# Performance work log

Measured on AMD Instinct MI355X. Metric: run time of the kernel, lower is better.

The kernel has to match this reference:

```python
import jax, jax.numpy as jnp
import numpy as np

B, S, D = 4, 4096, 200


def setup_inputs() -> dict:
    key = jax.random.key(0)
    ks = jax.random.split(key, 10)
    sc = 1.0 / np.sqrt(D)
    return {
        "modal1_input": jax.random.normal(ks[0], (B, S, D), dtype=jnp.float32),
        "modal2_input": jax.random.normal(ks[1], (B, S, D), dtype=jnp.float32),
        "Wq": jax.random.normal(ks[2], (D, D), dtype=jnp.float32) * sc,
        "bq": jnp.zeros((D,), dtype=jnp.float32),
        "Wk": jax.random.normal(ks[3], (D, D), dtype=jnp.float32) * sc,
        "bk": jnp.zeros((D,), dtype=jnp.float32),
        "Wv": jax.random.normal(ks[4], (D, D), dtype=jnp.float32) * sc,
        "bv": jnp.zeros((D,), dtype=jnp.float32),
        "Wo": jax.random.normal(ks[5], (D, D), dtype=jnp.float32) * sc,
        "bo": jnp.zeros((D,), dtype=jnp.float32),
    }


def _self_attend(x, Wq, bq, Wk, bk, Wv, bv):
    # torch nn.Linear: y = x @ W.T + b
    q = x @ Wq.T + bq  # [B,S,D]
    k = x @ Wk.T + bk
    v = x @ Wv.T + bv
    scale = 1.0 / jnp.sqrt(jnp.asarray(q.shape[-1], q.dtype))
    scores = jnp.einsum("bsd,btd->bst", q, k) * scale  # [B,S,S]
    w = jax.nn.softmax(scores, axis=-1)
    return jnp.einsum("bst,btd->bsd", w, v)


def reference(modal1_input, modal2_input, Wq, bq, Wk, bk, Wv, bv, Wo, bo):
    a1 = _self_attend(modal1_input, Wq, bq, Wk, bk, Wv, bv)
    a2 = _self_attend(modal2_input, Wq, bq, Wk, bk, Wv, bv)
    fused = a1 + a2
    return fused @ Wo.T + bo
```

## Files before the change

kernel.cpp:

```cpp
#include <hip/hip_runtime.h>

#define SLEN 4096
#define DIM  200
#define DP   224
#define DPL  232
#define VD   208
#define VTL  72
#define HKV  2048

typedef __bf16 bf16t;
typedef bf16t bf16x8 __attribute__((ext_vector_type(8)));
typedef float f32x4 __attribute__((ext_vector_type(4)));

static __device__ __forceinline__ f32x4 mfma16(bf16x8 a, bf16x8 b, f32x4 c) {
    return __builtin_amdgcn_mfma_f32_16x16x32_bf16(a, b, c, 0, 0, 0);
}

static __device__ __forceinline__ unsigned short f2bf(float f) {
    unsigned int u = __float_as_uint(f);
    u += 0x7FFFu + ((u >> 16) & 1u);
    return (unsigned short)(u >> 16);
}

static __device__ __forceinline__ float bf2f(unsigned short s) {
    return __uint_as_float((unsigned)s << 16);
}

static __device__ __forceinline__ uint2 pack4(float a, float b, float c, float d) {
    uint2 r;
    r.x = (unsigned)f2bf(a) | ((unsigned)f2bf(b) << 16);
    r.y = (unsigned)f2bf(c) | ((unsigned)f2bf(d) << 16);
    return r;
}

__global__ __launch_bounds__(256, 2)
void proj_kernel(const float* __restrict__ x1, const float* __restrict__ x2,
                 const float* __restrict__ Wq, const float* __restrict__ bq,
                 const float* __restrict__ Wk, const float* __restrict__ bk,
                 const float* __restrict__ Wv, const float* __restrict__ bv,
                 unsigned short* __restrict__ Qg, unsigned short* __restrict__ Kg,
                 unsigned short* __restrict__ Vtg)
{
    __shared__ unsigned short x_lds[64 * DPL];
    __shared__ unsigned short w_lds[64 * DPL];
    __shared__ unsigned short vt_lds[64 * 66];

    const int tid = threadIdx.x;
    const int mod = blockIdx.x >> 8;
    const int rb  = blockIdx.x & 255;
    const int r0  = rb * 64;
    const int bidx = r0 >> 12;
    const int s0  = r0 & 4095;
    const int unit = mod * 4 + bidx;
    const float* __restrict__ x = mod ? x2 : x1;

    for (int i = tid; i < 3200; i += 256) {
        int r = i / 50, c = i % 50;
        const float4 v = *(const float4*)(x + (size_t)(r0 + r) * DIM + c * 4);
        *(uint2*)(x_lds + r * DPL + c * 4) = pack4(v.x, v.y, v.z, v.w);
    }
    {
        int r = tid >> 2, c4 = tid & 3;
        uint2 z = make_uint2(0u, 0u);
        *(uint2*)(x_lds + r * DPL + 200 + c4 * 4) = z;
        *(uint2*)(x_lds + r * DPL + 216 + c4 * 4) = z;
        *(uint2*)(w_lds + r * DPL + 200 + c4 * 4) = z;
        *(uint2*)(w_lds + r * DPL + 216 + c4 * 4) = z;
    }
    __syncthreads();

    const int wv = tid >> 6, lane = tid & 63, ln = lane & 15, h = lane >> 4;

    bf16x8 afrag[7];
    #pragma unroll
    for (int kk = 0; kk < 7; ++kk)
        afrag[kk] = *(const bf16x8*)(x_lds + (wv * 16 + ln) * DPL + kk * 32 + 8 * h);

    for (int mmat = 0; mmat < 3; ++mmat) {
        const float* W  = (mmat == 0) ? Wq : (mmat == 1 ? Wk : Wv);
        const float* bi = (mmat == 0) ? bq : (mmat == 1 ? bk : bv);
        for (int t = 0; t < 4; ++t) {
            for (int i = tid; i < 3200; i += 256) {
                int r = i / 50, c = i % 50;
                int og = t * 64 + r;
                uint2 val = make_uint2(0u, 0u);
                if (og < DIM) {
                    const float4 v = *(const float4*)(W + (size_t)og * DIM + c * 4);
                    val = pack4(v.x, v.y, v.z, v.w);
                }
                *(uint2*)(w_lds + r * DPL + c * 4) = val;
            }
            __syncthreads();

            f32x4 acc[4];
            #pragma unroll
            for (int sub = 0; sub < 4; ++sub) acc[sub] = (f32x4){0.f, 0.f, 0.f, 0.f};
            #pragma unroll
            for (int kk = 0; kk < 7; ++kk) {
                #pragma unroll
                for (int sub = 0; sub < 4; ++sub) {
                    bf16x8 bfrag = *(const bf16x8*)(w_lds + (sub * 16 + ln) * DPL + kk * 32 + 8 * h);
                    acc[sub] = mfma16(afrag[kk], bfrag, acc[sub]);
                }
            }

            if (mmat < 2) {
                unsigned short* dst = (mmat == 0) ? Qg : Kg;
                #pragma unroll
                for (int sub = 0; sub < 4; ++sub) {
                    int og = t * 64 + sub * 16 + ln;
                    if (og < DIM) {
                        float bias = bi[og];
                        #pragma unroll
                        for (int r = 0; r < 4; ++r) {
                            int srow = s0 + wv * 16 + 4 * h + r;
                            dst[((size_t)unit * SLEN + srow) * DP + og] = f2bf(acc[sub][r] + bias);
                        }
                    }
                }
                __syncthreads();
            } else {
                #pragma unroll
                for (int sub = 0; sub < 4; ++sub) {
                    int og = t * 64 + sub * 16 + ln;
                    float bias = (og < DIM) ? bi[og] : 0.f;
                    #pragma unroll
                    for (int r = 0; r < 4; ++r) {
                        float val = (og < DIM) ? (acc[sub][r] + bias) : 0.f;
                        vt_lds[(wv * 16 + 4 * h + r) * 66 + sub * 16 + ln] = f2bf(val);
                    }
                }
                __syncthreads();
                for (int p = 0; p < 2; ++p) {
                    int idx = p * 256 + tid;
                    int dl = idx >> 3, cc = idx & 7;
                    int og = t * 64 + dl;
                    if (og < VD) {
                        unsigned short tmp[8];
                        #pragma unroll
                        for (int j = 0; j < 8; ++j)
                            tmp[j] = vt_lds[(cc * 8 + j) * 66 + dl];
                        *(uint4*)(Vtg + ((size_t)unit * VD + og) * SLEN + s0 + cc * 8) = *(uint4*)tmp;
                    }
                }
                __syncthreads();
            }
        }
    }
}

__global__ __launch_bounds__(512, 4)
void attn_kernel(const unsigned short* __restrict__ Qg,
                 const unsigned short* __restrict__ Kg,
                 const unsigned short* __restrict__ Vtg,
                 unsigned short* __restrict__ Ap,
                 float2* __restrict__ Mlg)
{
    __shared__ unsigned short k_lds[64 * DPL];
    __shared__ unsigned short vt_lds[VD * VTL];
    __shared__ unsigned short p_lds[8 * 16 * VTL];

    const int tid = threadIdx.x;
    const int u   = blockIdx.x & 7;
    const int qt  = (blockIdx.x >> 3) & 31;
    const int hf  = blockIdx.x >> 8;
    const int wv = tid >> 6, lane = tid & 63, ln = lane & 15, h = lane >> 4;
    const size_t ubase = (size_t)u * SLEN;

    bf16x8 qfrag[7];
    {
        const size_t qoff = (ubase + qt * 128 + wv * 16 + ln) * DP;
        #pragma unroll
        for (int kk = 0; kk < 7; ++kk)
            qfrag[kk] = *(const bf16x8*)(Qg + qoff + kk * 32 + 8 * h);
    }

    float mrun[4], lrun[4];
    #pragma unroll
    for (int r = 0; r < 4; ++r) { mrun[r] = -1e30f; lrun[r] = 0.f; }
    f32x4 acc[13];
    #pragma unroll
    for (int d = 0; d < 13; ++d) acc[d] = (f32x4){0.f, 0.f, 0.f, 0.f};

    const float scale = 0.07071067811865475f;
    const int t_beg = hf * HKV;

    for (int t0 = t_beg; t0 < t_beg + HKV; t0 += 64) {
        #pragma unroll
        for (int it = 0; it < 4; ++it) {
            int i = it * 512 + tid;
            if (i < 1792) {
                int r = i / 28, c = i % 28;
                *(uint4*)(k_lds + r * DPL + c * 8) =
                    *(const uint4*)(Kg + (ubase + t0 + r) * DP + c * 8);
            }
            if (i < 1664) {
                int r = i >> 3, c = i & 7;
                *(uint4*)(vt_lds + r * VTL + c * 8) =
                    *(const uint4*)(Vtg + ((size_t)u * VD + r) * SLEN + t0 + c * 8);
            }
        }
        __syncthreads();

        f32x4 sc[4];
        #pragma unroll
        for (int sub = 0; sub < 4; ++sub) sc[sub] = (f32x4){0.f, 0.f, 0.f, 0.f};
        #pragma unroll
        for (int kk = 0; kk < 7; ++kk) {
            #pragma unroll
            for (int sub = 0; sub < 4; ++sub) {
                bf16x8 bfrag = *(const bf16x8*)(k_lds + (sub * 16 + ln) * DPL + kk * 32 + 8 * h);
                sc[sub] = mfma16(qfrag[kk], bfrag, sc[sub]);
            }
        }

        float mxs[4];
        #pragma unroll
        for (int r = 0; r < 4; ++r) {
            float mx = fmaxf(fmaxf(sc[0][r], sc[1][r]), fmaxf(sc[2][r], sc[3][r]));
            mx = fmaxf(mx, __shfl_xor(mx, 1));
            mx = fmaxf(mx, __shfl_xor(mx, 2));
            mx = fmaxf(mx, __shfl_xor(mx, 4));
            mx = fmaxf(mx, __shfl_xor(mx, 8));
            mxs[r] = mx * scale;
        }

        int need = (mxs[0] > mrun[0] + 8.f) | (mxs[1] > mrun[1] + 8.f) |
                   (mxs[2] > mrun[2] + 8.f) | (mxs[3] > mrun[3] + 8.f);
        if (__any(need)) {
            #pragma unroll
            for (int r = 0; r < 4; ++r) {
                float mnew = fmaxf(mrun[r], mxs[r]);
                float alpha = __expf(mrun[r] - mnew);
                lrun[r] *= alpha;
                #pragma unroll
                for (int d = 0; d < 13; ++d) acc[d][r] *= alpha;
                mrun[r] = mnew;
            }
        }

        #pragma unroll
        for (int r = 0; r < 4; ++r) {
            float rsum = 0.f;
            #pragma unroll
            for (int sub = 0; sub < 4; ++sub) {
                float p = __expf(sc[sub][r] * scale - mrun[r]);
                rsum += p;
                p_lds[wv * (16 * VTL) + (4 * h + r) * VTL + sub * 16 + ln] = f2bf(p);
            }
            rsum += __shfl_xor(rsum, 1);
            rsum += __shfl_xor(rsum, 2);
            rsum += __shfl_xor(rsum, 4);
            rsum += __shfl_xor(rsum, 8);
            lrun[r] += rsum;
        }

        #pragma unroll
        for (int ks = 0; ks < 2; ++ks) {
            bf16x8 pfrag = *(const bf16x8*)(p_lds + wv * (16 * VTL) + ln * VTL + ks * 32 + 8 * h);
            #pragma unroll
            for (int d = 0; d < 13; ++d) {
                bf16x8 bfrag = *(const bf16x8*)(vt_lds + (d * 16 + ln) * VTL + ks * 32 + 8 * h);
                acc[d] = mfma16(pfrag, bfrag, acc[d]);
            }
        }
        __syncthreads();
    }

    const int slab = hf * 8 + u;
    unsigned short* Adst = Ap + (size_t)slab * SLEN * VD;
    #pragma unroll
    for (int r = 0; r < 4; ++r) {
        int srow = qt * 128 + wv * 16 + 4 * h + r;
        #pragma unroll
        for (int d = 0; d < 13; ++d)
            Adst[(size_t)srow * VD + d * 16 + ln] = f2bf(acc[d][r]);
        if (ln == 0)
            Mlg[(size_t)slab * SLEN + srow] = make_float2(mrun[r], lrun[r]);
    }
}

__global__ __launch_bounds__(256, 2)
void out_kernel(const unsigned short* __restrict__ Ap,
                const float2* __restrict__ Mlg,
                const float* __restrict__ Wo,
                const float* __restrict__ bo, float* __restrict__ out)
{
    __shared__ unsigned short a_lds[64 * DPL];
    __shared__ unsigned short w_lds[64 * DPL];

    const int tid = threadIdx.x;
    const int r0 = blockIdx.x * 64;
    const int bidx = r0 >> 12;
    const int s0 = r0 & 4095;

    const unsigned short* A1a = Ap + (size_t)(bidx)      * SLEN * VD;
    const unsigned short* A1b = Ap + (size_t)(8 + bidx)  * SLEN * VD;
    const unsigned short* A2a = Ap + (size_t)(4 + bidx)  * SLEN * VD;
    const unsigned short* A2b = Ap + (size_t)(12 + bidx) * SLEN * VD;
    const float2* M1a = Mlg + (size_t)(bidx)      * SLEN;
    const float2* M1b = Mlg + (size_t)(8 + bidx)  * SLEN;
    const float2* M2a = Mlg + (size_t)(4 + bidx)  * SLEN;
    const float2* M2b = Mlg + (size_t)(12 + bidx) * SLEN;

    for (int i = tid; i < 3200; i += 256) {
        int r = i / 50, c = i % 50;
        int srow = s0 + r;
        size_t off = (size_t)srow * VD + c * 4;

        float2 ml1a = M1a[srow], ml1b = M1b[srow];
        float2 ml2a = M2a[srow], ml2b = M2b[srow];
        float M1 = fmaxf(ml1a.x, ml1b.x);
        float w1a = __expf(ml1a.x - M1), w1b = __expf(ml1b.x - M1);
        float inv1 = 1.f / (ml1a.y * w1a + ml1b.y * w1b);
        float M2 = fmaxf(ml2a.x, ml2b.x);
        float w2a = __expf(ml2a.x - M2), w2b = __expf(ml2b.x - M2);
        float inv2 = 1.f / (ml2a.y * w2a + ml2b.y * w2b);

        uint2 pa = *(const uint2*)(A1a + off);
        uint2 pb = *(const uint2*)(A1b + off);
        uint2 qa = *(const uint2*)(A2a + off);
        uint2 qb = *(const uint2*)(A2b + off);

        float f[4];
        f[0] = (bf2f((unsigned short)(pa.x & 0xffff)) * w1a + bf2f((unsigned short)(pb.x & 0xffff)) * w1b) * inv1
             + (bf2f((unsigned short)(qa.x & 0xffff)) * w2a + bf2f((unsigned short)(qb.x & 0xffff)) * w2b) * inv2;
        f[1] = (bf2f((unsigned short)(pa.x >> 16))    * w1a + bf2f((unsigned short)(pb.x >> 16))    * w1b) * inv1
             + (bf2f((unsigned short)(qa.x >> 16))    * w2a + bf2f((unsigned short)(qb.x >> 16))    * w2b) * inv2;
        f[2] = (bf2f((unsigned short)(pa.y & 0xffff)) * w1a + bf2f((unsigned short)(pb.y & 0xffff)) * w1b) * inv1
             + (bf2f((unsigned short)(qa.y & 0xffff)) * w2a + bf2f((unsigned short)(qb.y & 0xffff)) * w2b) * inv2;
        f[3] = (bf2f((unsigned short)(pa.y >> 16))    * w1a + bf2f((unsigned short)(pb.y >> 16))    * w1b) * inv1
             + (bf2f((unsigned short)(qa.y >> 16))    * w2a + bf2f((unsigned short)(qb.y >> 16))    * w2b) * inv2;

        *(uint2*)(a_lds + r * DPL + c * 4) = pack4(f[0], f[1], f[2], f[3]);
    }
    {
        int r = tid >> 2, c4 = tid & 3;
        uint2 z = make_uint2(0u, 0u);
        *(uint2*)(a_lds + r * DPL + 200 + c4 * 4) = z;
        *(uint2*)(a_lds + r * DPL + 216 + c4 * 4) = z;
        *(uint2*)(w_lds + r * DPL + 200 + c4 * 4) = z;
        *(uint2*)(w_lds + r * DPL + 216 + c4 * 4) = z;
    }
    __syncthreads();

    const int wv = tid >> 6, lane = tid & 63, ln = lane & 15, h = lane >> 4;
    bf16x8 afrag[7];
    #pragma unroll
    for (int kk = 0; kk < 7; ++kk)
        afrag[kk] = *(const bf16x8*)(a_lds + (wv * 16 + ln) * DPL + kk * 32 + 8 * h);

    for (int t = 0; t < 4; ++t) {
        for (int i = tid; i < 3200; i += 256) {
            int r = i / 50, c = i % 50;
            int og = t * 64 + r;
            uint2 val = make_uint2(0u, 0u);
            if (og < DIM) {
                const float4 v = *(const float4*)(Wo + (size_t)og * DIM + c * 4);
                val = pack4(v.x, v.y, v.z, v.w);
            }
            *(uint2*)(w_lds + r * DPL + c * 4) = val;
        }
        __syncthreads();

        f32x4 acc[4];
        #pragma unroll
        for (int sub = 0; sub < 4; ++sub) acc[sub] = (f32x4){0.f, 0.f, 0.f, 0.f};
        #pragma unroll
        for (int kk = 0; kk < 7; ++kk) {
            #pragma unroll
            for (int sub = 0; sub < 4; ++sub) {
                bf16x8 bfrag = *(const bf16x8*)(w_lds + (sub * 16 + ln) * DPL + kk * 32 + 8 * h);
                acc[sub] = mfma16(afrag[kk], bfrag, acc[sub]);
            }
        }

        #pragma unroll
        for (int sub = 0; sub < 4; ++sub) {
            int og = t * 64 + sub * 16 + ln;
            if (og < DIM) {
                float bias = bo[og];
                #pragma unroll
                for (int r = 0; r < 4; ++r) {
                    int row = r0 + wv * 16 + 4 * h + r;
                    out[(size_t)row * DIM + og] = acc[sub][r] + bias;
                }
            }
        }
        __syncthreads();
    }
}

extern "C" void kernel_launch(void* const* d_in, const int* in_sizes, int n_in,
                              void* d_out, int out_size, void* d_ws, size_t ws_size,
                              hipStream_t stream)
{
    const float* x1 = (const float*)d_in[0];
    const float* x2 = (const float*)d_in[1];
    const float* Wq = (const float*)d_in[2];
    const float* bq = (const float*)d_in[3];
    const float* Wk = (const float*)d_in[4];
    const float* bk = (const float*)d_in[5];
    const float* Wv = (const float*)d_in[6];
    const float* bv = (const float*)d_in[7];
    const float* Wo = (const float*)d_in[8];
    const float* bo = (const float*)d_in[9];

    unsigned short* Qg  = (unsigned short*)d_ws;
    unsigned short* Kg  = Qg + (size_t)8 * SLEN * DP;
    unsigned short* Vtg = Kg + (size_t)8 * SLEN * DP;
    unsigned short* Apg = Vtg + (size_t)8 * VD * SLEN;
    float2*         Mlg = (float2*)(Apg + (size_t)16 * SLEN * VD);

    proj_kernel<<<dim3(512), dim3(256), 0, stream>>>(x1, x2, Wq, bq, Wk, bk, Wv, bv,
                                                     Qg, Kg, Vtg);
    attn_kernel<<<dim3(512), dim3(512), 0, stream>>>(Qg, Kg, Vtg, Apg, Mlg);
    out_kernel<<<dim3(256), dim3(256), 0, stream>>>(Apg, Mlg, Wo, bo, (float*)d_out);
}
```

Baseline: 409.1 us.

## Give each attention wave two query tiles and precompute combine weights in out kernel

The attention kernel now runs 256 threads per block, and each wave handles 32 query rows as two 16-row MFMA tiles. Each K and V fragment read from LDS is reused across both tiles, halving LDS reads per MFMA. The cost is roughly double the accumulator and Q-fragment registers, plus fewer waves per block to hide latency. The output kernel now computes the per-row softmax combine weights once into shared memory and loads the attention partials with 16-byte reads instead of 8-byte reads.

```diff
diff --git a/kernel.cpp b/kernel.cpp
--- a/kernel.cpp
+++ b/kernel.cpp
@@ -149,7 +149,7 @@
     }
 }
 
-__global__ __launch_bounds__(512, 4)
+__global__ __launch_bounds__(256, 2)
 void attn_kernel(const unsigned short* __restrict__ Qg,
                  const unsigned short* __restrict__ Kg,
                  const unsigned short* __restrict__ Vtg,
@@ -158,7 +158,7 @@
 {
     __shared__ unsigned short k_lds[64 * DPL];
     __shared__ unsigned short vt_lds[VD * VTL];
-    __shared__ unsigned short p_lds[8 * 16 * VTL];
+    __shared__ unsigned short p_lds[128 * VTL];
 
     const int tid = threadIdx.x;
     const int u   = blockIdx.x & 7;
@@ -167,29 +167,34 @@
     const int wv = tid >> 6, lane = tid & 63, ln = lane & 15, h = lane >> 4;
     const size_t ubase = (size_t)u * SLEN;
 
-    bf16x8 qfrag[7];
-    {
-        const size_t qoff = (ubase + qt * 128 + wv * 16 + ln) * DP;
+    bf16x8 qfrag[2][7];
+    #pragma unroll
+    for (int mt = 0; mt < 2; ++mt) {
+        const size_t qoff = (ubase + qt * 128 + wv * 32 + mt * 16 + ln) * DP;
         #pragma unroll
         for (int kk = 0; kk < 7; ++kk)
-            qfrag[kk] = *(const bf16x8*)(Qg + qoff + kk * 32 + 8 * h);
-    }
-
-    float mrun[4], lrun[4];
-    #pragma unroll
-    for (int r = 0; r < 4; ++r) { mrun[r] = -1e30f; lrun[r] = 0.f; }
-    f32x4 acc[13];
-    #pragma unroll
-    for (int d = 0; d < 13; ++d) acc[d] = (f32x4){0.f, 0.f, 0.f, 0.f};
+            qfrag[mt][kk] = *(const bf16x8*)(Qg + qoff + kk * 32 + 8 * h);
+    }
+
+    float mrun[2][4], lrun[2][4];
+    #pragma unroll
+    for (int mt = 0; mt < 2; ++mt)
+        #pragma unroll
+        for (int r = 0; r < 4; ++r) { mrun[mt][r] = -1e30f; lrun[mt][r] = 0.f; }
+    f32x4 acc[2][13];
+    #pragma unroll
+    for (int mt = 0; mt < 2; ++mt)
+        #pragma unroll
+        for (int d = 0; d < 13; ++d) acc[mt][d] = (f32x4){0.f, 0.f, 0.f, 0.f};
 
     const float scale = 0.07071067811865475f;
     const int t_beg = hf * HKV;
 
     for (int t0 = t_beg; t0 < t_beg + HKV; t0 += 64) {
         #pragma unroll
-        for (int it = 0; it < 4; ++it) {
-            int i = it * 512 + tid;
-            if (i < 1792) {
+        for (int it = 0; it < 7; ++it) {
+            int i = it * 256 + tid;
+            {
                 int r = i / 28, c = i % 28;
                 *(uint4*)(k_lds + r * DPL + c * 8) =
                     *(const uint4*)(Kg + (ubase + t0 + r) * DP + c * 8);
@@ -202,66 +207,75 @@
         }
         __syncthreads();
 
-        f32x4 sc[4];
-        #pragma unroll
-        for (int sub = 0; sub < 4; ++sub) sc[sub] = (f32x4){0.f, 0.f, 0.f, 0.f};
+        f32x4 sc[2][4];
+        #pragma unroll
+        for (int mt = 0; mt < 2; ++mt)
+            #pragma unroll
+            for (int sub = 0; sub < 4; ++sub) sc[mt][sub] = (f32x4){0.f, 0.f, 0.f, 0.f};
         #pragma unroll
         for (int kk = 0; kk < 7; ++kk) {
             #pragma unroll
             for (int sub = 0; sub < 4; ++sub) {
                 bf16x8 bfrag = *(const bf16x8*)(k_lds + (sub * 16 + ln) * DPL + kk * 32 + 8 * h);
-                sc[sub] = mfma16(qfrag[kk], bfrag, sc[sub]);
-            }
-        }
-
-        float mxs[4];
-        #pragma unroll
-        for (int r = 0; r < 4; ++r) {
-            float mx = fmaxf(fmaxf(sc[0][r], sc[1][r]), fmaxf(sc[2][r], sc[3][r]));
-            mx = fmaxf(mx, __shfl_xor(mx, 1));
-            mx = fmaxf(mx, __shfl_xor(mx, 2));
-            mx = fmaxf(mx, __shfl_xor(mx, 4));
-            mx = fmaxf(mx, __shfl_xor(mx, 8));
-            mxs[r] = mx * scale;
-        }
-
-        int need = (mxs[0] > mrun[0] + 8.f) | (mxs[1] > mrun[1] + 8.f) |
-                   (mxs[2] > mrun[2] + 8.f) | (mxs[3] > mrun[3] + 8.f);
-        if (__any(need)) {
+                sc[0][sub] = mfma16(qfrag[0][kk], bfrag, sc[0][sub]);
+                sc[1][sub] = mfma16(qfrag[1][kk], bfrag, sc[1][sub]);
+            }
+        }
+
+        #pragma unroll
+        for (int mt = 0; mt < 2; ++mt) {
+            float mxs[4];
             #pragma unroll
             for (int r = 0; r < 4; ++r) {
-                float mnew = fmaxf(mrun[r], mxs[r]);
-                float alpha = __expf(mrun[r] - mnew);
-                lrun[r] *= alpha;
-                #pragma unroll
-                for (int d = 0; d < 13; ++d) acc[d][r] *= alpha;
-                mrun[r] = mnew;
-            }
-        }
-
-        #pragma unroll
-        for (int r = 0; r < 4; ++r) {
-            float rsum = 0.f;
-            #pragma unroll
-            for (int sub = 0; sub < 4; ++sub) {
-                float p = __expf(sc[sub][r] * scale - mrun[r]);
-                rsum += p;
-                p_lds[wv * (16 * VTL) + (4 * h + r) * VTL + sub * 16 + ln] = f2bf(p);
-            }
-            rsum += __shfl_xor(rsum, 1);
-            rsum += __shfl_xor(rsum, 2);
-            rsum += __shfl_xor(rsum, 4);
-            rsum += __shfl_xor(rsum, 8);
-            lrun[r] += rsum;
+                float mx = fmaxf(fmaxf(sc[mt][0][r], sc[mt][1][r]),
+                                 fmaxf(sc[mt][2][r], sc[mt][3][r]));
+                mx = fmaxf(mx, __shfl_xor(mx, 1));
+                mx = fmaxf(mx, __shfl_xor(mx, 2));
+                mx = fmaxf(mx, __shfl_xor(mx, 4));
+                mx = fmaxf(mx, __shfl_xor(mx, 8));
+                mxs[r] = mx * scale;
+            }
+
+            int need = (mxs[0] > mrun[mt][0] + 8.f) | (mxs[1] > mrun[mt][1] + 8.f) |
+                       (mxs[2] > mrun[mt][2] + 8.f) | (mxs[3] > mrun[mt][3] + 8.f);
+            if (__any(need)) {
+                #pragma unroll
+                for (int r = 0; r < 4; ++r) {
+                    float mnew = fmaxf(mrun[mt][r], mxs[r]);
+                    float alpha = __expf(mrun[mt][r] - mnew);
+                    lrun[mt][r] *= alpha;
+                    #pragma unroll
+                    for (int d = 0; d < 13; ++d) acc[mt][d][r] *= alpha;
+                    mrun[mt][r] = mnew;
+                }
+            }
+
+            #pragma unroll
+            for (int r = 0; r < 4; ++r) {
+                float rsum = 0.f;
+                #pragma unroll
+                for (int sub = 0; sub < 4; ++sub) {
+                    float p = __expf(sc[mt][sub][r] * scale - mrun[mt][r]);
+                    rsum += p;
+                    p_lds[(wv * 32 + mt * 16 + 4 * h + r) * VTL + sub * 16 + ln] = f2bf(p);
+                }
+                rsum += __shfl_xor(rsum, 1);
+                rsum += __shfl_xor(rsum, 2);
+                rsum += __shfl_xor(rsum, 4);
+                rsum += __shfl_xor(rsum, 8);
+                lrun[mt][r] += rsum;
+            }
         }
 
         #pragma unroll
         for (int ks = 0; ks < 2; ++ks) {
-            bf16x8 pfrag = *(const bf16x8*)(p_lds + wv * (16 * VTL) + ln * VTL + ks * 32 + 8 * h);
+            bf16x8 pfrag0 = *(const bf16x8*)(p_lds + (wv * 32 + ln) * VTL + ks * 32 + 8 * h);
+            bf16x8 pfrag1 = *(const bf16x8*)(p_lds + (wv * 32 + 16 + ln) * VTL + ks * 32 + 8 * h);
             #pragma unroll
             for (int d = 0; d < 13; ++d) {
                 bf16x8 bfrag = *(const bf16x8*)(vt_lds + (d * 16 + ln) * VTL + ks * 32 + 8 * h);
-                acc[d] = mfma16(pfrag, bfrag, acc[d]);
+                acc[0][d] = mfma16(pfrag0, bfrag, acc[0][d]);
+                acc[1][d] = mfma16(pfrag1, bfrag, acc[1][d]);
             }
         }
         __syncthreads();
@@ -270,13 +284,16 @@
     const int slab = hf * 8 + u;
     unsigned short* Adst = Ap + (size_t)slab * SLEN * VD;
     #pragma unroll
-    for (int r = 0; r < 4; ++r) {
-        int srow = qt * 128 + wv * 16 + 4 * h + r;
-        #pragma unroll
-        for (int d = 0; d < 13; ++d)
-            Adst[(size_t)srow * VD + d * 16 + ln] = f2bf(acc[d][r]);
-        if (ln == 0)
-            Mlg[(size_t)slab * SLEN + srow] = make_float2(mrun[r], lrun[r]);
+    for (int mt = 0; mt < 2; ++mt) {
+        #pragma unroll
+        for (int r = 0; r < 4; ++r) {
+            int srow = qt * 128 + wv * 32 + mt * 16 + 4 * h + r;
+            #pragma unroll
+            for (int d = 0; d < 13; ++d)
+                Adst[(size_t)srow * VD + d * 16 + ln] = f2bf(acc[mt][d][r]);
+            if (ln == 0)
+                Mlg[(size_t)slab * SLEN + srow] = make_float2(mrun[mt][r], lrun[mt][r]);
+        }
     }
 }
 
@@ -288,6 +305,7 @@
 {
     __shared__ unsigned short a_lds[64 * DPL];
     __shared__ unsigned short w_lds[64 * DPL];
+    __shared__ float4 ml_s[64];
 
     const int tid = threadIdx.x;
     const int r0 = blockIdx.x * 64;
@@ -298,41 +316,46 @@
     const unsigned short* A1b = Ap + (size_t)(8 + bidx)  * SLEN * VD;
     const unsigned short* A2a = Ap + (size_t)(4 + bidx)  * SLEN * VD;
     const unsigned short* A2b = Ap + (size_t)(12 + bidx) * SLEN * VD;
-    const float2* M1a = Mlg + (size_t)(bidx)      * SLEN;
-    const float2* M1b = Mlg + (size_t)(8 + bidx)  * SLEN;
-    const float2* M2a = Mlg + (size_t)(4 + bidx)  * SLEN;
-    const float2* M2b = Mlg + (size_t)(12 + bidx) * SLEN;
-
-    for (int i = tid; i < 3200; i += 256) {
-        int r = i / 50, c = i % 50;
-        int srow = s0 + r;
-        size_t off = (size_t)srow * VD + c * 4;
-
-        float2 ml1a = M1a[srow], ml1b = M1b[srow];
-        float2 ml2a = M2a[srow], ml2b = M2b[srow];
+
+    if (tid < 64) {
+        int srow = s0 + tid;
+        float2 ml1a = Mlg[(size_t)(bidx)      * SLEN + srow];
+        float2 ml1b = Mlg[(size_t)(8 + bidx)  * SLEN + srow];
+        float2 ml2a = Mlg[(size_t)(4 + bidx)  * SLEN + srow];
+        float2 ml2b = Mlg[(size_t)(12 + bidx) * SLEN + srow];
         float M1 = fmaxf(ml1a.x, ml1b.x);
         float w1a = __expf(ml1a.x - M1), w1b = __expf(ml1b.x - M1);
         float inv1 = 1.f / (ml1a.y * w1a + ml1b.y * w1b);
         float M2 = fmaxf(ml2a.x, ml2b.x);
         float w2a = __expf(ml2a.x - M2), w2b = __expf(ml2b.x - M2);
         float inv2 = 1.f / (ml2a.y * w2a + ml2b.y * w2b);
-
-        uint2 pa = *(const uint2*)(A1a + off);
-        uint2 pb = *(const uint2*)(A1b + off);
-        uint2 qa = *(const uint2*)(A2a + off);
-        uint2 qb = *(const uint2*)(A2b + off);
-
-        float f[4];
-        f[0] = (bf2f((unsigned short)(pa.x & 0xffff)) * w1a + bf2f((unsigned short)(pb.x & 0xffff)) * w1b) * inv1
-             + (bf2f((unsigned short)(qa.x & 0xffff)) * w2a + bf2f((unsigned short)(qb.x & 0xffff)) * w2b) * inv2;
-        f[1] = (bf2f((unsigned short)(pa.x >> 16))    * w1a + bf2f((unsigned short)(pb.x >> 16))    * w1b) * inv1
-             + (bf2f((unsigned short)(qa.x >> 16))    * w2a + bf2f((unsigned short)(qb.x >> 16))    * w2b) * inv2;
-        f[2] = (bf2f((unsigned short)(pa.y & 0xffff)) * w1a + bf2f((unsigned short)(pb.y & 0xffff)) * w1b) * inv1
-             + (bf2f((unsigned short)(qa.y & 0xffff)) * w2a + bf2f((unsigned short)(qb.y & 0xffff)) * w2b) * inv2;
-        f[3] = (bf2f((unsigned short)(pa.y >> 16))    * w1a + bf2f((unsigned short)(pb.y >> 16))    * w1b) * inv1
-             + (bf2f((unsigned short)(qa.y >> 16))    * w2a + bf2f((unsigned short)(qb.y >> 16))    * w2b) * inv2;
-
-        *(uint2*)(a_lds + r * DPL + c * 4) = pack4(f[0], f[1], f[2], f[3]);
+        ml_s[tid] = make_float4(w1a * inv1, w1b * inv1, w2a * inv2, w2b * inv2);
+    }
+    __syncthreads();
+
+    for (int i = tid; i < 1600; i += 256) {
+        int r = i / 25, c = i % 25;
+        int srow = s0 + r;
+        size_t off = (size_t)srow * VD + c * 8;
+        float4 s = ml_s[r];
+
+        uint4 pa = *(const uint4*)(A1a + off);
+        uint4 pb = *(const uint4*)(A1b + off);
+        uint4 qa = *(const uint4*)(A2a + off);
+        uint4 qb = *(const uint4*)(A2b + off);
+
+        const unsigned* pau = &pa.x; const unsigned* pbu = &pb.x;
+        const unsigned* qau = &qa.x; const unsigned* qbu = &qb.x;
+        float f[8];
+        #pragma unroll
+        for (int j = 0; j < 4; ++j) {
+            f[2*j]   = (bf2f((unsigned short)(pau[j] & 0xffff)) * s.x + bf2f((unsigned short)(pbu[j] & 0xffff)) * s.y)
+                     + (bf2f((unsigned short)(qau[j] & 0xffff)) * s.z + bf2f((unsigned short)(qbu[j] & 0xffff)) * s.w);
+            f[2*j+1] = (bf2f((unsigned short)(pau[j] >> 16))    * s.x + bf2f((unsigned short)(pbu[j] >> 16))    * s.y)
+                     + (bf2f((unsigned short)(qau[j] >> 16))    * s.z + bf2f((unsigned short)(qbu[j] >> 16))    * s.w);
+        }
+        *(uint2*)(a_lds + r * DPL + c * 8)     = pack4(f[0], f[1], f[2], f[3]);
+        *(uint2*)(a_lds + r * DPL + c * 8 + 4) = pack4(f[4], f[5], f[6], f[7]);
     }
     {
         int r = tid >> 2, c4 = tid & 3;
@@ -414,6 +437,6 @@
 
     proj_kernel<<<dim3(512), dim3(256), 0, stream>>>(x1, x2, Wq, bq, Wk, bk, Wv, bv,
                                                      Qg, Kg, Vtg);
-    attn_kernel<<<dim3(512), dim3(512), 0, stream>>>(Qg, Kg, Vtg, Apg, Mlg);
+    attn_kernel<<<dim3(512), dim3(256), 0, stream>>>(Qg, Kg, Vtg, Apg, Mlg);
     out_kernel<<<dim3(256), dim3(256), 0, stream>>>(Apg, Mlg, Wo, bo, (float*)d_out);
 }
```

Result: slower. 456.1 us (+11.5%).

## Prefetch next K/V and weight tiles into registers across all three kernels

Applied to the files above, without the earlier changes.

Adds register-staged software prefetching in the projection, attention and output kernels. The next tile of K/V or weights is loaded from global memory into registers while the current tile is computed, then written to LDS after a barrier, so load latency is meant to overlap with MFMA work. Also adds s_setprio around the MFMA blocks, precomputes the per-row softmax merge weights once in LDS with wider 16-byte loads in the combine step, and switches bf16 conversion to the builtin cast. Costs extra VGPRs for the prefetch buffers, which may reduce occupancy given the launch bounds.

```diff
diff --git a/kernel.cpp b/kernel.cpp
--- a/kernel.cpp
+++ b/kernel.cpp
@@ -17,9 +17,7 @@
 }
 
 static __device__ __forceinline__ unsigned short f2bf(float f) {
-    unsigned int u = __float_as_uint(f);
-    u += 0x7FFFu + ((u >> 16) & 1u);
-    return (unsigned short)(u >> 16);
+    return __builtin_bit_cast(unsigned short, (__bf16)f);
 }
 
 static __device__ __forceinline__ float bf2f(unsigned short s) {
@@ -54,10 +52,15 @@
     const int unit = mod * 4 + bidx;
     const float* __restrict__ x = mod ? x2 : x1;
 
+    const float* const Ws[3] = {Wq, Wk, Wv};
+    const float* const bs[3] = {bq, bk, bv};
+
     for (int i = tid; i < 3200; i += 256) {
         int r = i / 50, c = i % 50;
         const float4 v = *(const float4*)(x + (size_t)(r0 + r) * DIM + c * 4);
         *(uint2*)(x_lds + r * DPL + c * 4) = pack4(v.x, v.y, v.z, v.w);
+        const float4 w = *(const float4*)(Wq + (size_t)r * DIM + c * 4);
+        *(uint2*)(w_lds + r * DPL + c * 4) = pack4(w.x, w.y, w.z, w.w);
     }
     {
         int r = tid >> 2, c4 = tid & 3;
@@ -76,75 +79,93 @@
     for (int kk = 0; kk < 7; ++kk)
         afrag[kk] = *(const bf16x8*)(x_lds + (wv * 16 + ln) * DPL + kk * 32 + 8 * h);
 
-    for (int mmat = 0; mmat < 3; ++mmat) {
-        const float* W  = (mmat == 0) ? Wq : (mmat == 1 ? Wk : Wv);
-        const float* bi = (mmat == 0) ? bq : (mmat == 1 ? bk : bv);
-        for (int t = 0; t < 4; ++t) {
-            for (int i = tid; i < 3200; i += 256) {
-                int r = i / 50, c = i % 50;
-                int og = t * 64 + r;
-                uint2 val = make_uint2(0u, 0u);
+    for (int p = 0; p < 12; ++p) {
+        const int mmat = p >> 2, t = p & 3;
+        const float* bi = bs[mmat];
+        const bool has_next = (p + 1) < 12;
+
+        float4 wf[13];
+        if (has_next) {
+            const int mm1 = (p + 1) >> 2, t1 = (p + 1) & 3;
+            const float* W1 = Ws[mm1];
+            #pragma unroll
+            for (int it = 0; it < 13; ++it) {
+                int i = it * 256 + tid;
+                wf[it] = make_float4(0.f, 0.f, 0.f, 0.f);
+                if (i < 3200) {
+                    int r = i / 50, c = i % 50;
+                    int og = t1 * 64 + r;
+                    if (og < DIM)
+                        wf[it] = *(const float4*)(W1 + (size_t)og * DIM + c * 4);
+                }
+            }
+        }
+
+        f32x4 acc[4];
+        #pragma unroll
+        for (int sub = 0; sub < 4; ++sub) acc[sub] = (f32x4){0.f, 0.f, 0.f, 0.f};
+        #pragma unroll
+        for (int kk = 0; kk < 7; ++kk) {
+            #pragma unroll
+            for (int sub = 0; sub < 4; ++sub) {
+                bf16x8 bfrag = *(const bf16x8*)(w_lds + (sub * 16 + ln) * DPL + kk * 32 + 8 * h);
+                acc[sub] = mfma16(afrag[kk], bfrag, acc[sub]);
+            }
+        }
+
+        if (mmat < 2) {
+            unsigned short* dst = (mmat == 0) ? Qg : Kg;
+            #pragma unroll
+            for (int sub = 0; sub < 4; ++sub) {
+                int og = t * 64 + sub * 16 + ln;
                 if (og < DIM) {
-                    const float4 v = *(const float4*)(W + (size_t)og * DIM + c * 4);
-                    val = pack4(v.x, v.y, v.z, v.w);
-                }
-                *(uint2*)(w_lds + r * DPL + c * 4) = val;
-            }
-            __syncthreads();
-
-            f32x4 acc[4];
-            #pragma unroll
-            for (int sub = 0; sub < 4; ++sub) acc[sub] = (f32x4){0.f, 0.f, 0.f, 0.f};
-            #pragma unroll
-            for (int kk = 0; kk < 7; ++kk) {
-                #pragma unroll
-                for (int sub = 0; sub < 4; ++sub) {
-                    bf16x8 bfrag = *(const bf16x8*)(w_lds + (sub * 16 + ln) * DPL + kk * 32 + 8 * h);
-                    acc[sub] = mfma16(afrag[kk], bfrag, acc[sub]);
-                }
-            }
-
-            if (mmat < 2) {
-                unsigned short* dst = (mmat == 0) ? Qg : Kg;
-                #pragma unroll
-                for (int sub = 0; sub < 4; ++sub) {
-                    int og = t * 64 + sub * 16 + ln;
-                    if (og < DIM) {
-                        float bias = bi[og];
-                        #pragma unroll
-                        for (int r = 0; r < 4; ++r) {
-                            int srow = s0 + wv * 16 + 4 * h + r;
-                            dst[((size_t)unit * SLEN + srow) * DP + og] = f2bf(acc[sub][r] + bias);
-                        }
-                    }
-                }
-                __syncthreads();
-            } else {
-                #pragma unroll
-                for (int sub = 0; sub < 4; ++sub) {
-                    int og = t * 64 + sub * 16 + ln;
-                    float bias = (og < DIM) ? bi[og] : 0.f;
+                    float bias = bi[og];
                     #pragma unroll
                     for (int r = 0; r < 4; ++r) {
-                        float val = (og < DIM) ? (acc[sub][r] + bias) : 0.f;
-                        vt_lds[(wv * 16 + 4 * h + r) * 66 + sub * 16 + ln] = f2bf(val);
+                        int srow = s0 + wv * 16 + 4 * h + r;
+                        dst[((size_t)unit * SLEN + srow) * DP + og] = f2bf(acc[sub][r] + bias);
                     }
                 }
-                __syncthreads();
-                for (int p = 0; p < 2; ++p) {
-                    int idx = p * 256 + tid;
-                    int dl = idx >> 3, cc = idx & 7;
-                    int og = t * 64 + dl;
-                    if (og < VD) {
-                        unsigned short tmp[8];
-                        #pragma unroll
-                        for (int j = 0; j < 8; ++j)
-                            tmp[j] = vt_lds[(cc * 8 + j) * 66 + dl];
-                        *(uint4*)(Vtg + ((size_t)unit * VD + og) * SLEN + s0 + cc * 8) = *(uint4*)tmp;
-                    }
-                }
-                __syncthreads();
-            }
+            }
+            __syncthreads();
+        } else {
+            #pragma unroll
+            for (int sub = 0; sub < 4; ++sub) {
+                int og = t * 64 + sub * 16 + ln;
+                float bias = (og < DIM) ? bi[og] : 0.f;
+                #pragma unroll
+                for (int r = 0; r < 4; ++r) {
+                    float val = (og < DIM) ? (acc[sub][r] + bias) : 0.f;
+                    vt_lds[(wv * 16 + 4 * h + r) * 66 + sub * 16 + ln] = f2bf(val);
+                }
+            }
+            __syncthreads();
+            for (int pp = 0; pp < 2; ++pp) {
+                int idx = pp * 256 + tid;
+                int dl = idx >> 3, cc = idx & 7;
+                int og = t * 64 + dl;
+                if (og < VD) {
+                    unsigned short tmp[8];
+                    #pragma unroll
+                    for (int j = 0; j < 8; ++j)
+                        tmp[j] = vt_lds[(cc * 8 + j) * 66 + dl];
+                    *(uint4*)(Vtg + ((size_t)unit * VD + og) * SLEN + s0 + cc * 8) = *(uint4*)tmp;
+                }
+            }
+            __syncthreads();
+        }
+
+        if (has_next) {
+            #pragma unroll
+            for (int it = 0; it < 13; ++it) {
+                int i = it * 256 + tid;
+                if (i < 3200) {
+                    int r = i / 50, c = i % 50;
+                    *(uint2*)(w_lds + r * DPL + c * 4) =
+                        pack4(wf[it].x, wf[it].y, wf[it].z, wf[it].w);
+                }
+            }
+            __syncthreads();
         }
     }
 }
@@ -184,27 +205,48 @@
 
     const float scale = 0.07071067811865475f;
     const int t_beg = hf * HKV;
-
-    for (int t0 = t_beg; t0 < t_beg + HKV; t0 += 64) {
-        #pragma unroll
-        for (int it = 0; it < 4; ++it) {
-            int i = it * 512 + tid;
-            if (i < 1792) {
-                int r = i / 28, c = i % 28;
-                *(uint4*)(k_lds + r * DPL + c * 8) =
-                    *(const uint4*)(Kg + (ubase + t0 + r) * DP + c * 8);
-            }
-            if (i < 1664) {
-                int r = i >> 3, c = i & 7;
-                *(uint4*)(vt_lds + r * VTL + c * 8) =
-                    *(const uint4*)(Vtg + ((size_t)u * VD + r) * SLEN + t0 + c * 8);
-            }
-        }
-        __syncthreads();
+    const int t_end = t_beg + HKV;
+
+    #pragma unroll
+    for (int it = 0; it < 4; ++it) {
+        int i = it * 512 + tid;
+        if (i < 1792) {
+            int r = i / 28, c = i % 28;
+            *(uint4*)(k_lds + r * DPL + c * 8) =
+                *(const uint4*)(Kg + (ubase + t_beg + r) * DP + c * 8);
+        }
+        if (i < 1664) {
+            int r = i >> 3, c = i & 7;
+            *(uint4*)(vt_lds + r * VTL + c * 8) =
+                *(const uint4*)(Vtg + ((size_t)u * VD + r) * SLEN + t_beg + c * 8);
+        }
+    }
+    __syncthreads();
+
+    for (int t0 = t_beg; t0 < t_end; t0 += 64) {
+        const bool has_next = (t0 + 64) < t_end;
+
+        uint4 pk[4], pv[4];
+        if (has_next) {
+            const int t1 = t0 + 64;
+            #pragma unroll
+            for (int it = 0; it < 4; ++it) {
+                int i = it * 512 + tid;
+                if (i < 1792) {
+                    int r = i / 28, c = i % 28;
+                    pk[it] = *(const uint4*)(Kg + (ubase + t1 + r) * DP + c * 8);
+                }
+                if (i < 1664) {
+                    int r = i >> 3, c = i & 7;
+                    pv[it] = *(const uint4*)(Vtg + ((size_t)u * VD + r) * SLEN + t1 + c * 8);
+                }
+            }
+        }
 
         f32x4 sc[4];
         #pragma unroll
         for (int sub = 0; sub < 4; ++sub) sc[sub] = (f32x4){0.f, 0.f, 0.f, 0.f};
+        __builtin_amdgcn_s_setprio(1);
         #pragma unroll
         for (int kk = 0; kk < 7; ++kk) {
             #pragma unroll
@@ -213,6 +255,7 @@
                 sc[sub] = mfma16(qfrag[kk], bfrag, sc[sub]);
             }
         }
+        __builtin_amdgcn_s_setprio(0);
 
         float mxs[4];
         #pragma unroll
@@ -255,6 +298,7 @@
             lrun[r] += rsum;
         }
 
+        __builtin_amdgcn_s_setprio(1);
         #pragma unroll
         for (int ks = 0; ks < 2; ++ks) {
             bf16x8 pfrag = *(const bf16x8*)(p_lds + wv * (16 * VTL) + ln * VTL + ks * 32 + 8 * h);
@@ -262,6 +306,24 @@
             for (int d = 0; d < 13; ++d) {
                 bf16x8 bfrag = *(const bf16x8*)(vt_lds + (d * 16 + ln) * VTL + ks * 32 + 8 * h);
                 acc[d] = mfma16(pfrag, bfrag, acc[d]);
+            }
+        }
+        __builtin_amdgcn_s_setprio(0);
+
+        __syncthreads();
+
+        if (has_next) {
+            #pragma unroll
+            for (int it = 0; it < 4; ++it) {
+                int i = it * 512 + tid;
+                if (i < 1792) {
+                    int r = i / 28, c = i % 28;
+                    *(uint4*)(k_lds + r * DPL + c * 8) = pk[it];
+                }
+                if (i < 1664) {
+                    int r = i >> 3, c = i & 7;
+                    *(uint4*)(vt_lds + r * VTL + c * 8) = pv[it];
+                }
             }
         }
         __syncthreads();
@@ -288,6 +350,7 @@
 {
     __shared__ unsigned short a_lds[64 * DPL];
     __shared__ unsigned short w_lds[64 * DPL];
+    __shared__ float4 ml_s[64];
 
     const int tid = threadIdx.x;
     const int r0 = blockIdx.x * 64;
@@ -298,41 +361,51 @@
     const unsigned short* A1b = Ap + (size_t)(8 + bidx)  * SLEN * VD;
     const unsigned short* A2a = Ap + (size_t)(4 + bidx)  * SLEN * VD;
     const unsigned short* A2b = Ap + (size_t)(12 + bidx) * SLEN * VD;
-    const float2* M1a = Mlg + (size_t)(bidx)      * SLEN;
-    const float2* M1b = Mlg + (size_t)(8 + bidx)  * SLEN;
-    const float2* M2a = Mlg + (size_t)(4 + bidx)  * SLEN;
-    const float2* M2b = Mlg + (size_t)(12 + bidx) * SLEN;
-
-    for (int i = tid; i < 3200; i += 256) {
-        int r = i / 50, c = i % 50;
-        int srow = s0 + r;
-        size_t off = (size_t)srow * VD + c * 4;
-
-        float2 ml1a = M1a[srow], ml1b = M1b[srow];
-        float2 ml2a = M2a[srow], ml2b = M2b[srow];
+
+    if (tid < 64) {
+        int srow = s0 + tid;
+        float2 ml1a = Mlg[(size_t)(bidx)      * SLEN + srow];
+        float2 ml1b = Mlg[(size_t)(8 + bidx)  * SLEN + srow];
+        float2 ml2a = Mlg[(size_t)(4 + bidx)  * SLEN + srow];
+        float2 ml2b = Mlg[(size_t)(12 + bidx) * SLEN + srow];
         float M1 = fmaxf(ml1a.x, ml1b.x);
         float w1a = __expf(ml1a.x - M1), w1b = __expf(ml1b.x - M1);
         float inv1 = 1.f / (ml1a.y * w1a + ml1b.y * w1b);
         float M2 = fmaxf(ml2a.x, ml2b.x);
         float w2a = __expf(ml2a.x - M2), w2b = __expf(ml2b.x - M2);
         float inv2 = 1.f / (ml2a.y * w2a + ml2b.y * w2b);
-
-        uint2 pa = *(const uint2*)(A1a + off);
-        uint2 pb = *(const uint2*)(A1b + off);
-        uint2 qa = *(const uint2*)(A2a + off);
-        uint2 qb = *(const uint2*)(A2b + off);
-
-        float f[4];
-        f[0] = (bf2f((unsigned short)(pa.x & 0xffff)) * w1a + bf2f((unsigned short)(pb.x & 0xffff)) * w1b) * inv1
-             + (bf2f((unsigned short)(qa.x & 0xffff)) * w2a + bf2f((unsigned short)(qb.x & 0xffff)) * w2b) * inv2;
-        f[1] = (bf2f((unsigned short)(pa.x >> 16))    * w1a + bf2f((unsigned short)(pb.x >> 16))    * w1b) * inv1
-             + (bf2f((unsigned short)(qa.x >> 16))    * w2a + bf2f((unsigned short)(qb.x >> 16))    * w2b) * inv2;
-        f[2] = (bf2f((unsigned short)(pa.y & 0xffff)) * w1a + bf2f((unsigned short)(pb.y & 0xffff)) * w1b) * inv1
-             + (bf2f((unsigned short)(qa.y & 0xffff)) * w2a + bf2f((unsigned short)(qb.y & 0xffff)) * w2b) * inv2;
-        f[3] = (bf2f((unsigned short)(pa.y >> 16))    * w1a + bf2f((unsigned short)(pb.y >> 16))    * w1b) * inv1
-             + (bf2f((unsigned short)(qa.y >> 16))    * w2a + bf2f((unsigned short)(qb.y >> 16))    * w2b) * inv2;
-
-        *(uint2*)(a_lds + r * DPL + c * 4) = pack4(f[0], f[1], f[2], f[3]);
+        ml_s[tid] = make_float4(w1a * inv1, w1b * inv1, w2a * inv2, w2b * inv2);
+    }
+    __syncthreads();
+
+    for (int i = tid; i < 1600; i += 256) {
+        int r = i / 25, c = i % 25;
+        int srow = s0 + r;
+        size_t off = (size_t)srow * VD + c * 8;
+        float4 s = ml_s[r];
+
+        uint4 pa = *(const uint4*)(A1a + off);
+        uint4 pb = *(const uint4*)(A1b + off);
+        uint4 qa = *(const uint4*)(A2a + off);
+        uint4 qb = *(const uint4*)(A2b + off);
+
+        const unsigned* pau = &pa.x; const unsigned* pbu = &pb.x;
+        const unsigned* qau = &qa.x; const unsigned* qbu = &qb.x;
+        float f[8];
+        #pragma unroll
+        for (int j = 0; j < 4; ++j) {
+            f[2*j]   = (bf2f((unsigned short)(pau[j] & 0xffff)) * s.x + bf2f((unsigned short)(pbu[j] & 0xffff)) * s.y)
+                     + (bf2f((unsigned short)(qau[j] & 0xffff)) * s.z + bf2f((unsigned short)(qbu[j] & 0xffff)) * s.w);
+            f[2*j+1] = (bf2f((unsigned short)(pau[j] >> 16))    * s.x + bf2f((unsigned short)(pbu[j] >> 16))    * s.y)
+                     + (bf2f((unsigned short)(qau[j] >> 16))    * s.z + bf2f((unsigned short)(qbu[j] >> 16))    * s.w);
+        }
+        *(uint2*)(a_lds + r * DPL + c * 8)     = pack4(f[0], f[1], f[2], f[3]);
+        *(uint2*)(a_lds + r * DPL + c * 8 + 4) = pack4(f[4], f[5], f[6], f[7]);
+    }
+    for (int i = tid; i < 3200; i += 256) {
+        int r = i / 50, c = i % 50;
+        const float4 v = *(const float4*)(Wo + (size_t)r * DIM + c * 4);
+        *(uint2*)(w_lds + r * DPL + c * 4) = pack4(v.x, v.y, v.z, v.w);
     }
     {
         int r = tid >> 2, c4 = tid & 3;
@@ -351,17 +424,21 @@
         afrag[kk] = *(const bf16x8*)(a_lds + (wv * 16 + ln) * DPL + kk * 32 + 8 * h);
 
     for (int t = 0; t < 4; ++t) {
-        for (int i = tid; i < 3200; i += 256) {
-            int r = i / 50, c = i % 50;
-            int og = t * 64 + r;
-            uint2 val = make_uint2(0u, 0u);
-            if (og < DIM) {
-                const float4 v = *(const float4*)(Wo + (size_t)og * DIM + c * 4);
-                val = pack4(v.x, v.y, v.z, v.w);
-            }
-            *(uint2*)(w_lds + r * DPL + c * 4) = val;
-        }
-        __syncthreads();
+        const bool has_next = (t + 1) < 4;
+        float4 wf[13];
+        if (has_next) {
+            #pragma unroll
+            for (int it = 0; it < 13; ++it) {
+                int i = it * 256 + tid;
+                wf[it] = make_float4(0.f, 0.f, 0.f, 0.f);
+                if (i < 3200) {
+                    int r = i / 50, c = i % 50;
+                    int og = (t + 1) * 64 + r;
+                    if (og < DIM)
+                        wf[it] = *(const float4*)(Wo + (size_t)og * DIM + c * 4);
+                }
+            }
+        }
 
         f32x4 acc[4];
         #pragma unroll
@@ -388,6 +465,19 @@
             }
         }
         __syncthreads();
+
+        if (has_next) {
+            #pragma unroll
+            for (int it = 0; it < 13; ++it) {
+                int i = it * 256 + tid;
+                if (i < 3200) {
+                    int r = i / 50, c = i % 50;
+                    *(uint2*)(w_lds + r * DPL + c * 4) =
+                        pack4(wf[it].x, wf[it].y, wf[it].z, wf[it].w);
+                }
+            }
+            __syncthreads();
+        }
     }
 }
 
```

New measurement: 594.9 us. 45.4% more time.
